# Kernel tuning notes

Hardware: AMD Instinct MI355X
Metric: run time of the kernel (lower is better)

Reference implementation:

```python
import jax, jax.numpy as jnp
import numpy as np

N = 100000      # nodes
E = 3200000     # edges (avg degree 32)
F_IN = 16       # node_feature_size
R1, R2, R3 = 8, 16, 8   # gcn hidden sizes
N1 = 32                  # mlp hidden


def _lin(k, fan_in, shape):
    s = 1.0 / np.sqrt(fan_in)
    return jax.random.uniform(k, shape, minval=-s, maxval=s, dtype=jnp.float32)


def setup_inputs() -> dict:
    key = jax.random.key(0)
    ks = jax.random.split(key, 16)
    x = jax.random.normal(ks[0], (N, F_IN), dtype=jnp.float32)
    edge_index = jax.random.randint(ks[1], (2, E), 0, N, dtype=jnp.int64)
    return {
        "x": x,
        "edge_index": edge_index,
        # GraphConv k: out = mean_agg(x_j) @ W_rel + b + x @ W_root  (PyG GraphConv, lin_root bias=False)
        "W_rel1": _lin(ks[2], F_IN, (F_IN, R1)), "b1": _lin(ks[3], F_IN, (R1,)), "W_root1": _lin(ks[4], F_IN, (F_IN, R1)),
        "W_rel2": _lin(ks[5], R1, (R1, R2)),   "b2": _lin(ks[6], R1, (R2,)),   "W_root2": _lin(ks[7], R1, (R1, R2)),
        "W_rel3": _lin(ks[8], R2, (R2, R3)),   "b3": _lin(ks[9], R2, (R3,)),   "W_root3": _lin(ks[10], R2, (R2, R3)),
        "fc1_W": _lin(ks[11], R3, (R3, N1)), "fc1_b": _lin(ks[12], R3, (N1,)),
        "fc2_W": _lin(ks[13], N1, (N1, 1)),  "fc2_b": _lin(ks[14], N1, (1,)),
    }


def _graph_conv(x, src, dst, W_rel, b, W_root):
    # message: gather source features; aggregate: mean over incoming edges at dst
    n = x.shape[0]
    msg_sum = jax.ops.segment_sum(x[src], dst, num_segments=n)          # [N, F]
    cnt = jax.ops.segment_sum(jnp.ones(src.shape, x.dtype), dst, num_segments=n)
    mean = msg_sum / jnp.maximum(cnt, 1.0)[:, None]
    return mean @ W_rel + b + x @ W_root


def reference(x, edge_index, W_rel1, b1, W_root1, W_rel2, b2, W_root2,
              W_rel3, b3, W_root3, fc1_W, fc1_b, fc2_W, fc2_b):
    src, dst = edge_index[0], edge_index[1]
    h = jax.nn.sigmoid(_graph_conv(x, src, dst, W_rel1, b1, W_root1))
    h = jax.nn.sigmoid(_graph_conv(h, src, dst, W_rel2, b2, W_root2))
    h = jax.nn.sigmoid(_graph_conv(h, src, dst, W_rel3, b3, W_root3))
    h = jax.nn.sigmoid(h @ fc1_W + fc1_b)
    return h @ fc2_W + fc2_b   # [N, 1]
```

## Files before the change

kernel.cpp:

```cpp
#include <hip/hip_runtime.h>
#include <math.h>


#define CHUNK  8192
#define BW     128
#define MAXNB  800
#define MAXBLK 512
#define MAXB   5120

typedef _Float16 half8 __attribute__((ext_vector_type(8)));

static __device__ __forceinline__ float sigmoidf_(float x) {
    return 1.0f / (1.0f + expf(-x));
}

static __device__ __forceinline__ int scan256_excl(int v, int* s) {
    int tid = threadIdx.x;
    s[tid] = v;
    for (int off = 1; off < 256; off <<= 1) {
        __syncthreads();
        int t = (tid >= off) ? s[tid - off] : 0;
        __syncthreads();
        s[tid] += t;
    }
    __syncthreads();
    return s[tid] - v;
}

static __device__ __forceinline__ void gather_sum8(
    const half8* __restrict__ t, const int* __restrict__ csr,
    int rs, int from, int to, float* s) {
#pragma unroll
    for (int c = 0; c < 8; ++c) s[c] = 0.0f;
    int e = from;
    for (; e + 4 <= to; e += 4) {
        int4 ci = *(const int4*)(csr + rs + e);
        half8 v0 = t[ci.x]; half8 v1 = t[ci.y];
        half8 v2 = t[ci.z]; half8 v3 = t[ci.w];
#pragma unroll
        for (int c = 0; c < 8; ++c)
            s[c] += ((float)v0[c] + (float)v1[c]) + ((float)v2[c] + (float)v3[c]);
    }
    for (; e < to; ++e) {
        half8 v = t[csr[rs + e]];
#pragma unroll
        for (int c = 0; c < 8; ++c) s[c] += (float)v[c];
    }
}

static __device__ __forceinline__ void pair_gather_mean8(
    const half8* __restrict__ t, const int* __restrict__ csr,
    int rs, int d, int half, float* s) {
    int d1 = ((d >> 1) + 3) & ~3; if (d1 > d) d1 = d;
    int from = half ? d1 : 0;
    int to   = half ? d  : d1;
    gather_sum8(t, csr, rs, from, to, s);
#pragma unroll
    for (int c = 0; c < 8; ++c) s[c] += __shfl_xor(s[c], 1);
    float inv = 1.0f / (float)(d > 0 ? d : 1);
#pragma unroll
    for (int c = 0; c < 8; ++c) s[c] *= inv;
}

__global__ __launch_bounds__(256)
void transform1_kernel(const float* __restrict__ x, const float* __restrict__ Wrel,
                       const float* __restrict__ bias, const float* __restrict__ Wroot,
                       _Float16* __restrict__ t1, _Float16* __restrict__ z1, int n) {
    __shared__ float sWr[128], sWo[128], sb[8];
    int tid = threadIdx.x;
    if (tid < 128) { sWr[tid] = Wrel[tid]; sWo[tid] = Wroot[tid]; }
    if (tid < 8) sb[tid] = bias[tid];
    __syncthreads();
    int node = blockIdx.x * 256 + tid;
    if (node >= n) return;
    const float4* x4 = (const float4*)x;
    float xv[16];
#pragma unroll
    for (int k = 0; k < 4; ++k) {
        float4 v = x4[node * 4 + k];
        xv[4 * k] = v.x; xv[4 * k + 1] = v.y; xv[4 * k + 2] = v.z; xv[4 * k + 3] = v.w;
    }
    float ta[8], za[8];
#pragma unroll
    for (int j = 0; j < 8; ++j) { ta[j] = 0.0f; za[j] = sb[j]; }
#pragma unroll
    for (int f = 0; f < 16; ++f) {
        float xf = xv[f];
#pragma unroll
        for (int j = 0; j < 8; ++j) {
            ta[j] += xf * sWr[f * 8 + j];
            za[j] += xf * sWo[f * 8 + j];
        }
    }
    half8 th, zh;
#pragma unroll
    for (int j = 0; j < 8; ++j) { th[j] = (_Float16)ta[j]; zh[j] = (_Float16)za[j]; }
    ((half8*)t1)[node] = th;
    ((half8*)z1)[node] = zh;
}

__global__ __launch_bounds__(256)
void hist_kernel(const int* __restrict__ dst, int* __restrict__ counts_bm,
                 int E, int NB) {
    __shared__ int s_hist[MAXNB];
    int tid = threadIdx.x, blk = blockIdx.x;
    for (int i = tid; i < NB; i += 256) s_hist[i] = 0;
    __syncthreads();
    int base = blk * CHUNK;
    int cnt = E - base; if (cnt > CHUNK) cnt = CHUNK;
    if (cnt == CHUNK) {
        const int4* d4 = (const int4*)(dst + base);
#pragma unroll
        for (int k = 0; k < CHUNK / 1024; ++k) {
            int4 d = d4[k * 256 + tid];
            atomicAdd(&s_hist[d.x >> 7], 1);
            atomicAdd(&s_hist[d.y >> 7], 1);
            atomicAdd(&s_hist[d.z >> 7], 1);
            atomicAdd(&s_hist[d.w >> 7], 1);
        }
    } else {
        for (int i = tid; i < cnt; i += 256) atomicAdd(&s_hist[dst[base + i] >> 7], 1);
    }
    __syncthreads();
    for (int i = tid; i < NB; i += 256) counts_bm[blk * NB + i] = s_hist[i];
}

__global__ __launch_bounds__(256)
void btot_scan_kernel(const int* __restrict__ counts_bm, int* __restrict__ rawstart_t,
                      int* __restrict__ btot, int NB, int NBLK) {
    __shared__ int s_scan[256];
    __shared__ int s_c[MAXBLK];
    int b = blockIdx.x, tid = threadIdx.x;
    for (int i = tid; i < NBLK; i += 256) s_c[i] = counts_bm[i * NB + b];
    __syncthreads();
    int per = (NBLK + 255) / 256;
    int st = tid * per;
    int lsum = 0;
    for (int j = 0; j < per; ++j)
        if (st + j < NBLK) lsum += s_c[st + j];
    int excl = scan256_excl(lsum, s_scan);
    int run = excl;
    for (int j = 0; j < per; ++j)
        if (st + j < NBLK) { rawstart_t[b * NBLK + st + j] = run; run += s_c[st + j]; }
    if (tid == 255) btot[b] = s_scan[255];
}

__global__ __launch_bounds__(1024)
void bscan_kernel(const int* __restrict__ btot, int* __restrict__ bstart, int NB) {
    __shared__ int lds[1024];
    int tid = threadIdx.x;
    int v = (tid < NB) ? (((btot[tid] + 3) & ~3) + 512) : 0;
    lds[tid] = v;
    for (int off = 1; off < 1024; off <<= 1) {
        __syncthreads();
        int t = (tid >= off) ? lds[tid - off] : 0;
        __syncthreads();
        lds[tid] += t;
    }
    __syncthreads();
    if (tid < NB) bstart[tid] = lds[tid] - v;
}

__global__ __launch_bounds__(256)
void scatter_kernel(const int* __restrict__ src, const int* __restrict__ dst,
                    const int* __restrict__ rawstart_t, const int* __restrict__ bstart,
                    unsigned* __restrict__ stage, int E, int NB, int NBLK) {
    __shared__ int s_cur[MAXNB];
    int tid = threadIdx.x, blk = blockIdx.x;
    for (int i = tid; i < NB; i += 256)
        s_cur[i] = bstart[i] + rawstart_t[i * NBLK + blk];
    __syncthreads();
    int base = blk * CHUNK;
    int cnt = E - base; if (cnt > CHUNK) cnt = CHUNK;
    if (cnt == CHUNK) {
        const int4* d4 = (const int4*)(dst + base);
        const int4* s4 = (const int4*)(src + base);
#pragma unroll
        for (int k = 0; k < CHUNK / 1024; ++k) {
            int4 d = d4[k * 256 + tid];
            int4 s = s4[k * 256 + tid];
            int dd[4] = {d.x, d.y, d.z, d.w};
            int ss[4] = {s.x, s.y, s.z, s.w};
#pragma unroll
            for (int j = 0; j < 4; ++j) {
                int pos = atomicAdd(&s_cur[dd[j] >> 7], 1);
                stage[pos] = ((unsigned)(dd[j] & 127) << 17) | (unsigned)ss[j];
            }
        }
    } else {
        for (int i = tid; i < cnt; i += 256) {
            int d = dst[base + i], s = src[base + i];
            int pos = atomicAdd(&s_cur[d >> 7], 1);
            stage[pos] = ((unsigned)(d & 127) << 17) | (unsigned)s;
        }
    }
}

__global__ __launch_bounds__(256)
void bucket_csr_kernel(const unsigned* __restrict__ stage,
                       const int* __restrict__ bstart, const int* __restrict__ btot,
                       int* __restrict__ csr, int* __restrict__ deg,
                       int* __restrict__ rowstart, int N, int NB) {
    __shared__ unsigned s_p[MAXB];
    __shared__ int h[BW], hs[BW], curb[BW];
    int b = blockIdx.x, tid = threadIdx.x;
    int beg = bstart[b];
    int tot = btot[b]; if (tot > MAXB) tot = MAXB;

    const uint4* st4 = (const uint4*)(stage + beg);
    int n4 = tot >> 2;
    for (int i = tid; i < n4; i += 256) ((uint4*)s_p)[i] = st4[i];
    for (int i = (n4 << 2) + tid; i < tot; i += 256) s_p[i] = stage[beg + i];
    if (tid < BW) h[tid] = 0;
    __syncthreads();

    for (int i = tid; i < tot; i += 256) atomicAdd(&h[s_p[i] >> 17], 1);
    __syncthreads();
    if (tid == 0) {
        int acc = 0;
        for (int i = 0; i < BW; ++i) { hs[i] = acc; acc += (h[i] + 3) & ~3; }
    }
    __syncthreads();
    if (tid < BW) {
        curb[tid] = hs[tid];
        int node = b * BW + tid;
        if (node < N) { deg[node] = h[tid]; rowstart[node] = beg + hs[tid]; }
    }
    __syncthreads();
    for (int i = tid; i < tot; i += 256) {
        unsigned p = s_p[i];
        int pos = atomicAdd(&curb[p >> 17], 1);
        csr[beg + pos] = (int)(p & 0x1FFFF);
    }
}

__global__ __launch_bounds__(256)
void agg1_kernel(const _Float16* __restrict__ t1, const _Float16* __restrict__ z1,
                 const int* __restrict__ rowstart, const int* __restrict__ deg,
                 const int* __restrict__ csr, _Float16* __restrict__ h1, int n) {
    int idx = blockIdx.x * 256 + threadIdx.x;
    int node = idx >> 1, half = idx & 1;
    if (node >= n) return;
    float s[8];
    pair_gather_mean8((const half8*)t1, csr, rowstart[node], deg[node], half, s);
    if (half) return;
    half8 z = ((const half8*)z1)[node];
    half8 o;
#pragma unroll
    for (int c = 0; c < 8; ++c) o[c] = (_Float16)sigmoidf_(s[c] + (float)z[c]);
    ((half8*)h1)[node] = o;
}

__global__ __launch_bounds__(256)
void gcn2_fused_kernel(const _Float16* __restrict__ h1,
                       const int* __restrict__ rowstart, const int* __restrict__ deg,
                       const int* __restrict__ csr,
                       const float* __restrict__ W2r, const float* __restrict__ b2,
                       const float* __restrict__ W2o,
                       const float* __restrict__ W3r, const float* __restrict__ b3,
                       const float* __restrict__ W3o,
                       _Float16* __restrict__ t3, _Float16* __restrict__ z3, int n) {
    __shared__ float sW2r[128], sW2o[128], sW3r[128], sW3o[128], sb2[16], sb3[8];
    int tid = threadIdx.x;
    if (tid < 128) {
        sW2r[tid] = W2r[tid]; sW2o[tid] = W2o[tid];
        sW3r[tid] = W3r[tid]; sW3o[tid] = W3o[tid];
    }
    if (tid < 16) sb2[tid] = b2[tid];
    if (tid < 8) sb3[tid] = b3[tid];
    __syncthreads();
    int idx = blockIdx.x * 256 + tid;
    int node = idx >> 1, half = idx & 1;
    if (node >= n) return;

    float m[8];
    pair_gather_mean8((const half8*)h1, csr, rowstart[node], deg[node], half, m);
    half8 sf = ((const half8*)h1)[node];
    float x8[8];
#pragma unroll
    for (int c = 0; c < 8; ++c) x8[c] = (float)sf[c];

    float v16[16];
#pragma unroll
    for (int j = 0; j < 16; ++j) {
        float a = sb2[j];
#pragma unroll
        for (int f = 0; f < 8; ++f)
            a += m[f] * sW2r[f * 16 + j] + x8[f] * sW2o[f * 16 + j];
        v16[j] = sigmoidf_(a);
    }
    float ta[8], za[8];
#pragma unroll
    for (int j = 0; j < 8; ++j) { ta[j] = 0.0f; za[j] = sb3[j]; }
#pragma unroll
    for (int f = 0; f < 16; ++f) {
        float hv = v16[f];
#pragma unroll
        for (int j = 0; j < 8; ++j) {
            ta[j] += hv * sW3r[f * 8 + j];
            za[j] += hv * sW3o[f * 8 + j];
        }
    }
    if (half) return;
    half8 th, zh;
#pragma unroll
    for (int j = 0; j < 8; ++j) { th[j] = (_Float16)ta[j]; zh[j] = (_Float16)za[j]; }
    ((half8*)t3)[node] = th;
    ((half8*)z3)[node] = zh;
}

__global__ __launch_bounds__(256)
void agg3_mlp_kernel(const _Float16* __restrict__ t3, const _Float16* __restrict__ z3,
                     const int* __restrict__ rowstart, const int* __restrict__ deg,
                     const int* __restrict__ csr,
                     const float* __restrict__ fc1W, const float* __restrict__ fc1b,
                     const float* __restrict__ fc2W, const float* __restrict__ fc2b,
                     float* __restrict__ out, int n) {
    __shared__ float sW1[256], sb1[32], sW2[32];
    __shared__ float sb2_;
    int tid = threadIdx.x;
    if (tid < 256) sW1[tid] = fc1W[tid];
    if (tid < 32) { sb1[tid] = fc1b[tid]; sW2[tid] = fc2W[tid]; }
    if (tid == 0) sb2_ = fc2b[0];
    __syncthreads();
    int idx = blockIdx.x * 256 + tid;
    int node = idx >> 1, half = idx & 1;
    if (node >= n) return;

    float s[8];
    pair_gather_mean8((const half8*)t3, csr, rowstart[node], deg[node], half, s);
    half8 z = ((const half8*)z3)[node];
    float h[8];
#pragma unroll
    for (int c = 0; c < 8; ++c) h[c] = sigmoidf_(s[c] + (float)z[c]);

    float acc = sb2_;
#pragma unroll
    for (int j = 0; j < 32; ++j) {
        float a = sb1[j];
#pragma unroll
        for (int f = 0; f < 8; ++f) a += h[f] * sW1[f * 32 + j];
        acc += sW2[j] * sigmoidf_(a);
    }
    if (half == 0) out[node] = acc;
}

extern "C" void kernel_launch(void* const* d_in, const int* in_sizes, int n_in,
                              void* d_out, int out_size, void* d_ws, size_t ws_size,
                              hipStream_t stream) {
    const float* x      = (const float*)d_in[0];
    const int*   ei     = (const int*)d_in[1];
    const float* Wrel1  = (const float*)d_in[2];
    const float* b1     = (const float*)d_in[3];
    const float* Wroot1 = (const float*)d_in[4];
    const float* Wrel2  = (const float*)d_in[5];
    const float* b2     = (const float*)d_in[6];
    const float* Wroot2 = (const float*)d_in[7];
    const float* Wrel3  = (const float*)d_in[8];
    const float* b3     = (const float*)d_in[9];
    const float* Wroot3 = (const float*)d_in[10];
    const float* fc1W   = (const float*)d_in[11];
    const float* fc1b   = (const float*)d_in[12];
    const float* fc2W   = (const float*)d_in[13];
    const float* fc2b   = (const float*)d_in[14];
    float* out = (float*)d_out;

    const int N = in_sizes[0] / 16;
    const int E = in_sizes[1] / 2;
    const int* e_src = ei;
    const int* e_dst = ei + E;

    const int NB   = (N + BW - 1) / BW;
    const int NBLK = (E + CHUNK - 1) / CHUNK;
    const int nbN  = (N + 255) / 256;
    const int nbP  = (2 * N + 255) / 256;

    char* ws = (char*)d_ws;
    size_t off = 0;
    auto alloc = [&](size_t bytes) { char* p = ws + off; off += (bytes + 15) & ~size_t(15); return p; };
    unsigned* stage    = (unsigned*)alloc(((size_t)E + (size_t)NB * 516 + 64) * 4);
    int* csr           = (int*)alloc(((size_t)E + (size_t)NB * 516 + 64) * 4);
    int* counts_bm     = (int*)alloc((size_t)NBLK * NB * 4);
    int* rawstart_t    = (int*)alloc((size_t)NB * NBLK * 4);
    int* btot          = (int*)alloc((size_t)NB * 4);
    int* bstart        = (int*)alloc((size_t)NB * 4);
    int* deg           = (int*)alloc((size_t)N * 4);
    int* rowstart      = (int*)alloc((size_t)N * 4);
    _Float16* t1       = (_Float16*)alloc((size_t)N * 8 * 2);
    _Float16* z1       = (_Float16*)alloc((size_t)N * 8 * 2);
    _Float16* h1       = (_Float16*)alloc((size_t)N * 8 * 2);
    _Float16* t3       = (_Float16*)alloc((size_t)N * 8 * 2);
    _Float16* z3       = (_Float16*)alloc((size_t)N * 8 * 2);

    transform1_kernel<<<nbN, 256, 0, stream>>>(x, Wrel1, b1, Wroot1, t1, z1, N);

    hist_kernel<<<NBLK, 256, 0, stream>>>(e_dst, counts_bm, E, NB);
    btot_scan_kernel<<<NB, 256, 0, stream>>>(counts_bm, rawstart_t, btot, NB, NBLK);
    bscan_kernel<<<1, 1024, 0, stream>>>(btot, bstart, NB);
    scatter_kernel<<<NBLK, 256, 0, stream>>>(e_src, e_dst, rawstart_t, bstart, stage, E, NB, NBLK);
    bucket_csr_kernel<<<NB, 256, 0, stream>>>(stage, bstart, btot, csr, deg, rowstart, N, NB);

    agg1_kernel<<<nbP, 256, 0, stream>>>(t1, z1, rowstart, deg, csr, h1, N);
    gcn2_fused_kernel<<<nbP, 256, 0, stream>>>(h1, rowstart, deg, csr,
                                               Wrel2, b2, Wroot2, Wrel3, b3, Wroot3, t3, z3, N);
    agg3_mlp_kernel<<<nbP, 256, 0, stream>>>(t3, z3, rowstart, deg, csr,
                                             fc1W, fc1b, fc2W, fc2b, out, N);
}
```

Measured before the change: 255.8 us.

## Fuse CSR build phases, use fixed bucket regions, and quad-thread gathers

Merges the layer-1 transform and histogram into one launch. The bucket prefix-scan kernel is removed by giving each bucket a fixed-size region in the staging buffer. Bucket width and chunk size grow to 512 nodes and 16384 edges. Layer-1 aggregation is fused into the CSR build kernel, and layers 2 and 3 use four threads per node instead of two. This cuts launches and passes over global memory, but fixed regions waste memory and tot is clamped to MAXB, so a bucket holding more than 17856 edges would silently drop edges (average is about 16.4K).

After: 238.1 us. 1.07x faster.

```diff
diff --git a/kernel.cpp b/kernel.cpp
--- a/kernel.cpp
+++ b/kernel.cpp
@@ -2,11 +2,9 @@
 #include <math.h>
 
 
-#define CHUNK  8192
-#define BW     128
-#define MAXNB  800
-#define MAXBLK 512
-#define MAXB   5120
+#define CHUNK  16384
+#define BW     512
+#define MAXB   17856
 
 typedef _Float16 half8 __attribute__((ext_vector_type(8)));
 
@@ -48,127 +46,105 @@
     }
 }
 
-static __device__ __forceinline__ void pair_gather_mean8(
+static __device__ __forceinline__ void quad_gather_mean8(
     const half8* __restrict__ t, const int* __restrict__ csr,
-    int rs, int d, int half, float* s) {
-    int d1 = ((d >> 1) + 3) & ~3; if (d1 > d) d1 = d;
-    int from = half ? d1 : 0;
-    int to   = half ? d  : d1;
+    int rs, int d, int q, float* s) {
+    int qs = ((d + 15) >> 4) << 2;
+    int from = q * qs; if (from > d) from = d;
+    int to = from + qs; if (to > d) to = d;
     gather_sum8(t, csr, rs, from, to, s);
 #pragma unroll
     for (int c = 0; c < 8; ++c) s[c] += __shfl_xor(s[c], 1);
+#pragma unroll
+    for (int c = 0; c < 8; ++c) s[c] += __shfl_xor(s[c], 2);
     float inv = 1.0f / (float)(d > 0 ? d : 1);
 #pragma unroll
     for (int c = 0; c < 8; ++c) s[c] *= inv;
 }
 
-__global__ __launch_bounds__(256)
-void transform1_kernel(const float* __restrict__ x, const float* __restrict__ Wrel,
-                       const float* __restrict__ bias, const float* __restrict__ Wroot,
-                       _Float16* __restrict__ t1, _Float16* __restrict__ z1, int n) {
+__global__ __launch_bounds__(512)
+void setup_kernel(const float* __restrict__ x, const float* __restrict__ Wrel,
+                  const float* __restrict__ bias, const float* __restrict__ Wroot,
+                  _Float16* __restrict__ t1, _Float16* __restrict__ z1,
+                  const int* __restrict__ dst, int* __restrict__ counts_bm,
+                  int N, int E, int NB, int nbT) {
     __shared__ float sWr[128], sWo[128], sb[8];
-    int tid = threadIdx.x;
-    if (tid < 128) { sWr[tid] = Wrel[tid]; sWo[tid] = Wroot[tid]; }
-    if (tid < 8) sb[tid] = bias[tid];
-    __syncthreads();
-    int node = blockIdx.x * 256 + tid;
-    if (node >= n) return;
-    const float4* x4 = (const float4*)x;
-    float xv[16];
-#pragma unroll
-    for (int k = 0; k < 4; ++k) {
-        float4 v = x4[node * 4 + k];
-        xv[4 * k] = v.x; xv[4 * k + 1] = v.y; xv[4 * k + 2] = v.z; xv[4 * k + 3] = v.w;
-    }
-    float ta[8], za[8];
-#pragma unroll
-    for (int j = 0; j < 8; ++j) { ta[j] = 0.0f; za[j] = sb[j]; }
-#pragma unroll
-    for (int f = 0; f < 16; ++f) {
-        float xf = xv[f];
-#pragma unroll
-        for (int j = 0; j < 8; ++j) {
-            ta[j] += xf * sWr[f * 8 + j];
-            za[j] += xf * sWo[f * 8 + j];
-        }
-    }
-    half8 th, zh;
-#pragma unroll
-    for (int j = 0; j < 8; ++j) { th[j] = (_Float16)ta[j]; zh[j] = (_Float16)za[j]; }
-    ((half8*)t1)[node] = th;
-    ((half8*)z1)[node] = zh;
-}
-
-__global__ __launch_bounds__(256)
-void hist_kernel(const int* __restrict__ dst, int* __restrict__ counts_bm,
-                 int E, int NB) {
-    __shared__ int s_hist[MAXNB];
+    __shared__ int s_hist[BW];
     int tid = threadIdx.x, blk = blockIdx.x;
-    for (int i = tid; i < NB; i += 256) s_hist[i] = 0;
-    __syncthreads();
-    int base = blk * CHUNK;
-    int cnt = E - base; if (cnt > CHUNK) cnt = CHUNK;
-    if (cnt == CHUNK) {
-        const int4* d4 = (const int4*)(dst + base);
-#pragma unroll
-        for (int k = 0; k < CHUNK / 1024; ++k) {
-            int4 d = d4[k * 256 + tid];
-            atomicAdd(&s_hist[d.x >> 7], 1);
-            atomicAdd(&s_hist[d.y >> 7], 1);
-            atomicAdd(&s_hist[d.z >> 7], 1);
-            atomicAdd(&s_hist[d.w >> 7], 1);
-        }
+
+    if (blk < nbT) {
+        if (tid < 128) { sWr[tid] = Wrel[tid]; sWo[tid] = Wroot[tid]; }
+        if (tid >= 128 && tid < 136) sb[tid - 128] = bias[tid - 128];
+        __syncthreads();
+        int node = blk * 512 + tid;
+        if (node >= N) return;
+        const float4* x4 = (const float4*)x;
+        float xv[16];
+#pragma unroll
+        for (int k = 0; k < 4; ++k) {
+            float4 v = x4[node * 4 + k];
+            xv[4 * k] = v.x; xv[4 * k + 1] = v.y; xv[4 * k + 2] = v.z; xv[4 * k + 3] = v.w;
+        }
+        float ta[8], za[8];
+#pragma unroll
+        for (int j = 0; j < 8; ++j) { ta[j] = 0.0f; za[j] = sb[j]; }
+#pragma unroll
+        for (int f = 0; f < 16; ++f) {
+            float xf = xv[f];
+#pragma unroll
+            for (int j = 0; j < 8; ++j) {
+                ta[j] += xf * sWr[f * 8 + j];
+                za[j] += xf * sWo[f * 8 + j];
+            }
+        }
+        half8 th, zh;
+#pragma unroll
+        for (int j = 0; j < 8; ++j) { th[j] = (_Float16)ta[j]; zh[j] = (_Float16)za[j]; }
+        ((half8*)t1)[node] = th;
+        ((half8*)z1)[node] = zh;
     } else {
-        for (int i = tid; i < cnt; i += 256) atomicAdd(&s_hist[dst[base + i] >> 7], 1);
-    }
-    __syncthreads();
-    for (int i = tid; i < NB; i += 256) counts_bm[blk * NB + i] = s_hist[i];
+        int chunk = blk - nbT;
+        int base = chunk * CHUNK;
+        int cnt = E - base; if (cnt > CHUNK) cnt = CHUNK;
+        for (int i = tid; i < NB; i += 512) s_hist[i] = 0;
+        __syncthreads();
+        if (cnt == CHUNK) {
+            const int4* d4 = (const int4*)(dst + base);
+#pragma unroll
+            for (int k = 0; k < CHUNK / 2048; ++k) {
+                int4 d = d4[k * 512 + tid];
+                atomicAdd(&s_hist[d.x >> 9], 1);
+                atomicAdd(&s_hist[d.y >> 9], 1);
+                atomicAdd(&s_hist[d.z >> 9], 1);
+                atomicAdd(&s_hist[d.w >> 9], 1);
+            }
+        } else {
+            for (int i = tid; i < cnt; i += 512) atomicAdd(&s_hist[dst[base + i] >> 9], 1);
+        }
+        __syncthreads();
+        for (int i = tid; i < NB; i += 512) counts_bm[chunk * NB + i] = s_hist[i];
+    }
 }
 
 __global__ __launch_bounds__(256)
 void btot_scan_kernel(const int* __restrict__ counts_bm, int* __restrict__ rawstart_t,
                       int* __restrict__ btot, int NB, int NBLK) {
-    __shared__ int s_scan[256];
-    __shared__ int s_c[MAXBLK];
+    __shared__ int s[256];
     int b = blockIdx.x, tid = threadIdx.x;
-    for (int i = tid; i < NBLK; i += 256) s_c[i] = counts_bm[i * NB + b];
-    __syncthreads();
-    int per = (NBLK + 255) / 256;
-    int st = tid * per;
-    int lsum = 0;
-    for (int j = 0; j < per; ++j)
-        if (st + j < NBLK) lsum += s_c[st + j];
-    int excl = scan256_excl(lsum, s_scan);
-    int run = excl;
-    for (int j = 0; j < per; ++j)
-        if (st + j < NBLK) { rawstart_t[b * NBLK + st + j] = run; run += s_c[st + j]; }
-    if (tid == 255) btot[b] = s_scan[255];
-}
-
-__global__ __launch_bounds__(1024)
-void bscan_kernel(const int* __restrict__ btot, int* __restrict__ bstart, int NB) {
-    __shared__ int lds[1024];
-    int tid = threadIdx.x;
-    int v = (tid < NB) ? (((btot[tid] + 3) & ~3) + 512) : 0;
-    lds[tid] = v;
-    for (int off = 1; off < 1024; off <<= 1) {
-        __syncthreads();
-        int t = (tid >= off) ? lds[tid - off] : 0;
-        __syncthreads();
-        lds[tid] += t;
-    }
-    __syncthreads();
-    if (tid < NB) bstart[tid] = lds[tid] - v;
-}
-
-__global__ __launch_bounds__(256)
+    int v = (tid < NBLK) ? counts_bm[tid * NB + b] : 0;
+    int excl = scan256_excl(v, s);
+    if (tid < NBLK) rawstart_t[b * NBLK + tid] = excl;
+    if (tid == 255) btot[b] = s[255];
+}
+
+__global__ __launch_bounds__(512)
 void scatter_kernel(const int* __restrict__ src, const int* __restrict__ dst,
-                    const int* __restrict__ rawstart_t, const int* __restrict__ bstart,
-                    unsigned* __restrict__ stage, int E, int NB, int NBLK) {
-    __shared__ int s_cur[MAXNB];
+                    const int* __restrict__ rawstart_t, unsigned* __restrict__ stage,
+                    int E, int NB, int NBLK, int region) {
+    __shared__ int s_cur[BW];
     int tid = threadIdx.x, blk = blockIdx.x;
-    for (int i = tid; i < NB; i += 256)
-        s_cur[i] = bstart[i] + rawstart_t[i * NBLK + blk];
+    for (int i = tid; i < NB; i += 512)
+        s_cur[i] = i * region + rawstart_t[i * NBLK + blk];
     __syncthreads();
     int base = blk * CHUNK;
     int cnt = E - base; if (cnt > CHUNK) cnt = CHUNK;
@@ -176,79 +152,83 @@
         const int4* d4 = (const int4*)(dst + base);
         const int4* s4 = (const int4*)(src + base);
 #pragma unroll
-        for (int k = 0; k < CHUNK / 1024; ++k) {
-            int4 d = d4[k * 256 + tid];
-            int4 s = s4[k * 256 + tid];
+        for (int k = 0; k < CHUNK / 2048; ++k) {
+            int4 d = d4[k * 512 + tid];
+            int4 s = s4[k * 512 + tid];
             int dd[4] = {d.x, d.y, d.z, d.w};
             int ss[4] = {s.x, s.y, s.z, s.w};
 #pragma unroll
             for (int j = 0; j < 4; ++j) {
-                int pos = atomicAdd(&s_cur[dd[j] >> 7], 1);
-                stage[pos] = ((unsigned)(dd[j] & 127) << 17) | (unsigned)ss[j];
+                int pos = atomicAdd(&s_cur[dd[j] >> 9], 1);
+                stage[pos] = ((unsigned)(dd[j] & 511) << 17) | (unsigned)ss[j];
             }
         }
     } else {
-        for (int i = tid; i < cnt; i += 256) {
+        for (int i = tid; i < cnt; i += 512) {
             int d = dst[base + i], s = src[base + i];
-            int pos = atomicAdd(&s_cur[d >> 7], 1);
-            stage[pos] = ((unsigned)(d & 127) << 17) | (unsigned)s;
-        }
-    }
-}
-
-__global__ __launch_bounds__(256)
-void bucket_csr_kernel(const unsigned* __restrict__ stage,
-                       const int* __restrict__ bstart, const int* __restrict__ btot,
-                       int* __restrict__ csr, int* __restrict__ deg,
-                       int* __restrict__ rowstart, int N, int NB) {
-    __shared__ unsigned s_p[MAXB];
-    __shared__ int h[BW], hs[BW], curb[BW];
+            int pos = atomicAdd(&s_cur[d >> 9], 1);
+            stage[pos] = ((unsigned)(d & 511) << 17) | (unsigned)s;
+        }
+    }
+}
+
+__global__ __launch_bounds__(512)
+void csr_agg1_kernel(const unsigned* __restrict__ stage, const int* __restrict__ btot,
+                     int* __restrict__ csr, int* __restrict__ deg,
+                     int* __restrict__ rowstart,
+                     const _Float16* __restrict__ t1, const _Float16* __restrict__ z1,
+                     _Float16* __restrict__ h1, int N, int region) {
+    __shared__ unsigned __attribute__((aligned(16))) s_p[MAXB];
+    __shared__ int h[BW], curb[BW];
     int b = blockIdx.x, tid = threadIdx.x;
-    int beg = bstart[b];
+    int beg = b * region;
     int tot = btot[b]; if (tot > MAXB) tot = MAXB;
 
     const uint4* st4 = (const uint4*)(stage + beg);
     int n4 = tot >> 2;
-    for (int i = tid; i < n4; i += 256) ((uint4*)s_p)[i] = st4[i];
-    for (int i = (n4 << 2) + tid; i < tot; i += 256) s_p[i] = stage[beg + i];
-    if (tid < BW) h[tid] = 0;
-    __syncthreads();
-
-    for (int i = tid; i < tot; i += 256) atomicAdd(&h[s_p[i] >> 17], 1);
-    __syncthreads();
-    if (tid == 0) {
-        int acc = 0;
-        for (int i = 0; i < BW; ++i) { hs[i] = acc; acc += (h[i] + 3) & ~3; }
-    }
-    __syncthreads();
-    if (tid < BW) {
-        curb[tid] = hs[tid];
-        int node = b * BW + tid;
-        if (node < N) { deg[node] = h[tid]; rowstart[node] = beg + hs[tid]; }
-    }
-    __syncthreads();
-    for (int i = tid; i < tot; i += 256) {
+    for (int i = tid; i < n4; i += 512) ((uint4*)s_p)[i] = st4[i];
+    for (int i = (n4 << 2) + tid; i < tot; i += 512) s_p[i] = stage[beg + i];
+    h[tid] = 0;
+    __syncthreads();
+
+    for (int i = tid; i < tot; i += 512) atomicAdd(&h[s_p[i] >> 17], 1);
+    __syncthreads();
+
+    int v = (h[tid] + 3) & ~3;
+    curb[tid] = v;
+    for (int off = 1; off < 512; off <<= 1) {
+        __syncthreads();
+        int t2 = (tid >= off) ? curb[tid - off] : 0;
+        __syncthreads();
+        curb[tid] += t2;
+    }
+    __syncthreads();
+    int myStart = curb[tid] - v;
+    int dg = h[tid];
+    __syncthreads();
+    curb[tid] = myStart;
+    int node = b * BW + tid;
+    if (node < N) { deg[node] = dg; rowstart[node] = beg + myStart; }
+    __syncthreads();
+
+    for (int i = tid; i < tot; i += 512) {
         unsigned p = s_p[i];
         int pos = atomicAdd(&curb[p >> 17], 1);
         csr[beg + pos] = (int)(p & 0x1FFFF);
     }
-}
-
-__global__ __launch_bounds__(256)
-void agg1_kernel(const _Float16* __restrict__ t1, const _Float16* __restrict__ z1,
-                 const int* __restrict__ rowstart, const int* __restrict__ deg,
-                 const int* __restrict__ csr, _Float16* __restrict__ h1, int n) {
-    int idx = blockIdx.x * 256 + threadIdx.x;
-    int node = idx >> 1, half = idx & 1;
-    if (node >= n) return;
-    float s[8];
-    pair_gather_mean8((const half8*)t1, csr, rowstart[node], deg[node], half, s);
-    if (half) return;
-    half8 z = ((const half8*)z1)[node];
-    half8 o;
-#pragma unroll
-    for (int c = 0; c < 8; ++c) o[c] = (_Float16)sigmoidf_(s[c] + (float)z[c]);
-    ((half8*)h1)[node] = o;
+    __syncthreads();
+
+    if (node < N) {
+        const half8* t = (const half8*)t1;
+        float s[8];
+        gather_sum8(t, csr, beg + myStart, 0, dg, s);
+        float inv = 1.0f / (float)(dg > 0 ? dg : 1);
+        half8 z = ((const half8*)z1)[node];
+        half8 o;
+#pragma unroll
+        for (int c = 0; c < 8; ++c) o[c] = (_Float16)sigmoidf_(s[c] * inv + (float)z[c]);
+        ((half8*)h1)[node] = o;
+    }
 }
 
 __global__ __launch_bounds__(256)
@@ -270,11 +250,11 @@
     if (tid < 8) sb3[tid] = b3[tid];
     __syncthreads();
     int idx = blockIdx.x * 256 + tid;
-    int node = idx >> 1, half = idx & 1;
+    int node = idx >> 2, q = idx & 3;
     if (node >= n) return;
 
     float m[8];
-    pair_gather_mean8((const half8*)h1, csr, rowstart[node], deg[node], half, m);
+    quad_gather_mean8((const half8*)h1, csr, rowstart[node], deg[node], q, m);
     half8 sf = ((const half8*)h1)[node];
     float x8[8];
 #pragma unroll
@@ -301,7 +281,7 @@
             za[j] += hv * sW3o[f * 8 + j];
         }
     }
-    if (half) return;
+    if (q) return;
     half8 th, zh;
 #pragma unroll
     for (int j = 0; j < 8; ++j) { th[j] = (_Float16)ta[j]; zh[j] = (_Float16)za[j]; }
@@ -324,11 +304,11 @@
     if (tid == 0) sb2_ = fc2b[0];
     __syncthreads();
     int idx = blockIdx.x * 256 + tid;
-    int node = idx >> 1, half = idx & 1;
+    int node = idx >> 2, q = idx & 3;
     if (node >= n) return;
 
     float s[8];
-    pair_gather_mean8((const half8*)t3, csr, rowstart[node], deg[node], half, s);
+    quad_gather_mean8((const half8*)t3, csr, rowstart[node], deg[node], q, s);
     half8 z = ((const half8*)z3)[node];
     float h[8];
 #pragma unroll
@@ -342,7 +322,7 @@
         for (int f = 0; f < 8; ++f) a += h[f] * sW1[f * 32 + j];
         acc += sW2[j] * sigmoidf_(a);
     }
-    if (half == 0) out[node] = acc;
+    if (q == 0) out[node] = acc;
 }
 
 extern "C" void kernel_launch(void* const* d_in, const int* in_sizes, int n_in,
@@ -372,18 +352,22 @@
 
     const int NB   = (N + BW - 1) / BW;
     const int NBLK = (E + CHUNK - 1) / CHUNK;
-    const int nbN  = (N + 255) / 256;
-    const int nbP  = (2 * N + 255) / 256;
+    const int nbT  = (N + 511) / 512;
+    const int nbQ  = (4 * N + 255) / 256;
+
+    int avgB = E / NB;
+    int region = avgB + avgB / 4 + 2048;
+    if (region < MAXB + 2048) region = MAXB + 2048;
+    region = (region + 3) & ~3;
 
     char* ws = (char*)d_ws;
     size_t off = 0;
     auto alloc = [&](size_t bytes) { char* p = ws + off; off += (bytes + 15) & ~size_t(15); return p; };
-    unsigned* stage    = (unsigned*)alloc(((size_t)E + (size_t)NB * 516 + 64) * 4);
-    int* csr           = (int*)alloc(((size_t)E + (size_t)NB * 516 + 64) * 4);
+    unsigned* stage    = (unsigned*)alloc((size_t)NB * region * 4);
+    int* csr           = (int*)alloc((size_t)NB * region * 4);
     int* counts_bm     = (int*)alloc((size_t)NBLK * NB * 4);
     int* rawstart_t    = (int*)alloc((size_t)NB * NBLK * 4);
     int* btot          = (int*)alloc((size_t)NB * 4);
-    int* bstart        = (int*)alloc((size_t)NB * 4);
     int* deg           = (int*)alloc((size_t)N * 4);
     int* rowstart      = (int*)alloc((size_t)N * 4);
     _Float16* t1       = (_Float16*)alloc((size_t)N * 8 * 2);
@@ -392,17 +376,14 @@
     _Float16* t3       = (_Float16*)alloc((size_t)N * 8 * 2);
     _Float16* z3       = (_Float16*)alloc((size_t)N * 8 * 2);
 
-    transform1_kernel<<<nbN, 256, 0, stream>>>(x, Wrel1, b1, Wroot1, t1, z1, N);
-
-    hist_kernel<<<NBLK, 256, 0, stream>>>(e_dst, counts_bm, E, NB);
+    setup_kernel<<<nbT + NBLK, 512, 0, stream>>>(x, Wrel1, b1, Wroot1, t1, z1,
+                                                 e_dst, counts_bm, N, E, NB, nbT);
     btot_scan_kernel<<<NB, 256, 0, stream>>>(counts_bm, rawstart_t, btot, NB, NBLK);
-    bscan_kernel<<<1, 1024, 0, stream>>>(btot, bstart, NB);
-    scatter_kernel<<<NBLK, 256, 0, stream>>>(e_src, e_dst, rawstart_t, bstart, stage, E, NB, NBLK);
-    bucket_csr_kernel<<<NB, 256, 0, stream>>>(stage, bstart, btot, csr, deg, rowstart, N, NB);
-
-    agg1_kernel<<<nbP, 256, 0, stream>>>(t1, z1, rowstart, deg, csr, h1, N);
-    gcn2_fused_kernel<<<nbP, 256, 0, stream>>>(h1, rowstart, deg, csr,
+    scatter_kernel<<<NBLK, 512, 0, stream>>>(e_src, e_dst, rawstart_t, stage, E, NB, NBLK, region);
+    csr_agg1_kernel<<<NB, 512, 0, stream>>>(stage, btot, csr, deg, rowstart,
+                                            t1, z1, h1, N, region);
+    gcn2_fused_kernel<<<nbQ, 256, 0, stream>>>(h1, rowstart, deg, csr,
                                                Wrel2, b2, Wroot2, Wrel3, b3, Wroot3, t3, z3, N);
-    agg3_mlp_kernel<<<nbP, 256, 0, stream>>>(t3, z3, rowstart, deg, csr,
+    agg3_mlp_kernel<<<nbQ, 256, 0, stream>>>(t3, z3, rowstart, deg, csr,
                                              fc1W, fc1b, fc2W, fc2b, out, N);
 }
```
